# Kernel tuning notes

Measured on AMD Instinct MI355X. Metric: run time of the kernel, lower is better.

Reference implementation:

```python
import jax, jax.numpy as jnp
import numpy as np

# ---- sRGB <-> CIELAB (D65) helpers, matching standard torch lab2rgb/rgb2lab ----
_RGB2XYZ = jnp.array([[0.412453, 0.357580, 0.180423],
                      [0.212671, 0.715160, 0.072169],
                      [0.019334, 0.119193, 0.950227]], dtype=jnp.float32)
_XYZ2RGB = jnp.array([[ 3.2404542, -1.5371385, -0.4985314],
                      [-0.9692660,  1.8760108,  0.0415560],
                      [ 0.0556434, -0.2040259,  1.0572252]], dtype=jnp.float32)
_WHITE = jnp.array([0.95047, 1.0, 1.08883], dtype=jnp.float32)
_EPS = 0.008856      # (6/29)^3
_KAPPA = 7.787

def _srgb_to_linear(c):
    safe = jnp.maximum(c, 0.04045)
    return jnp.where(c <= 0.04045, c / 12.92, ((safe + 0.055) / 1.055) ** 2.4)

def _linear_to_srgb(c):
    safe = jnp.maximum(c, 0.0031308)
    return jnp.where(c <= 0.0031308, 12.92 * c, 1.055 * safe ** (1.0 / 2.4) - 0.055)

def rgb2lab(rgb):
    lin = _srgb_to_linear(rgb)                      # [N,3]
    xyz = (lin @ _RGB2XYZ.T) / _WHITE               # [N,3]
    safe = jnp.maximum(xyz, _EPS)
    f = jnp.where(xyz > _EPS, jnp.cbrt(safe), _KAPPA * xyz + 16.0 / 116.0)
    fx, fy, fz = f[..., 0], f[..., 1], f[..., 2]
    L = 116.0 * fy - 16.0
    a = 500.0 * (fx - fy)
    b = 200.0 * (fy - fz)
    return jnp.stack([L, a, b], axis=-1)

def lab2rgb(lab):
    L, a, b = lab[..., 0], lab[..., 1], lab[..., 2]
    fy = (L + 16.0) / 116.0
    fx = fy + a / 500.0
    fz = fy - b / 200.0
    f = jnp.stack([fx, fy, fz], axis=-1)
    f3 = f ** 3
    t = jnp.where(f3 > _EPS, f3, (f - 16.0 / 116.0) / _KAPPA)
    xyz = t * _WHITE
    lin = xyz @ _XYZ2RGB.T
    return _linear_to_srgb(lin)

def _forward(x, w_seq1, b_seq1, w_seq2, b_seq2, w_lin, b_lin,
             w_comb, b_comb, w_logd, b_logd, w_final, b_final):
    # lab branch
    seq = jnp.tanh(x @ w_seq1 + b_seq1) @ w_seq2 + b_seq2        # [N,3]
    lin = x @ w_lin + b_lin                                      # [N,3]
    final_lab = jnp.concatenate([lin, seq], axis=-1) @ w_comb + b_comb
    # log-density branch
    x_rgb = lab2rgb(x)
    log_density = -jnp.log10(x_rgb)
    model_processed = log_density @ w_logd + b_logd
    back_to_lab = rgb2lab(10.0 ** model_processed)
    return jnp.concatenate([final_lab, back_to_lab], axis=-1) @ w_final + b_final


def setup_inputs() -> dict:
    key = jax.random.key(0)
    ks = jax.random.split(key, 13)
    N, H = 2_097_152, 64

    def lin_init(kw, kb, fan_in, fan_out):
        bound = 1.0 / np.sqrt(fan_in)
        w = jax.random.uniform(kw, (fan_in, fan_out), minval=-bound, maxval=bound, dtype=jnp.float32)
        b = jax.random.uniform(kb, (fan_out,), minval=-bound, maxval=bound, dtype=jnp.float32)
        return w, b

    # valid Lab inputs: sample sRGB away from 0/1 then convert
    rgb = jax.random.uniform(ks[0], (N, 3), minval=0.05, maxval=0.95, dtype=jnp.float32)
    x = rgb2lab(rgb)

    kk = jax.random.split(ks[1], 12)
    w_seq1, b_seq1 = lin_init(kk[0], kk[1], 3, H)
    w_seq2, b_seq2 = lin_init(kk[2], kk[3], H, 3)
    w_lin, b_lin = lin_init(kk[4], kk[5], 3, 3)
    w_comb, b_comb = lin_init(kk[6], kk[7], 6, 3)
    w_logd, b_logd = lin_init(kk[8], kk[9], 3, 3)
    w_final, b_final = lin_init(kk[10], kk[11], 6, 3)
    return {"x": x,
            "w_seq1": w_seq1, "b_seq1": b_seq1, "w_seq2": w_seq2, "b_seq2": b_seq2,
            "w_lin": w_lin, "b_lin": b_lin, "w_comb": w_comb, "b_comb": b_comb,
            "w_logd": w_logd, "b_logd": b_logd, "w_final": w_final, "b_final": b_final}


def reference(x, w_seq1, b_seq1, w_seq2, b_seq2, w_lin, b_lin,
              w_comb, b_comb, w_logd, b_logd, w_final, b_final):
    return _forward(x, w_seq1, b_seq1, w_seq2, b_seq2, w_lin, b_lin,
                    w_comb, b_comb, w_logd, b_logd, w_final, b_final)
```

## Files before the change

kernel.cpp:

```cpp
#include <hip/hip_runtime.h>

typedef float    v2f __attribute__((ext_vector_type(2)));
typedef _Float16 v2h __attribute__((ext_vector_type(2)));

__device__ __forceinline__ float fexp2(float x) { return __builtin_amdgcn_exp2f(x); }
__device__ __forceinline__ float flog2(float x) { return __builtin_amdgcn_logf(x); }
__device__ __forceinline__ float ffma (float a, float b, float c) { return __builtin_fmaf(a, b, c); }
__device__ __forceinline__ v2f  splat(float s) { v2f v; v.x = s; v.y = s; return v; }
__device__ __forceinline__ v2f  pkfma(v2f a, v2f b, v2f c) { return __builtin_elementwise_fma(a, b, c); }
__device__ __forceinline__ v2h  splath(float s) { v2h v; v.x = (_Float16)s; v.y = (_Float16)s; return v; }
__device__ __forceinline__ v2h  pkfmah(v2h a, v2h b, v2h c) { return __builtin_elementwise_fma(a, b, c); }
__device__ __forceinline__ v2h  cvt_pk(float a, float b) {
    return __builtin_bit_cast(v2h, __builtin_amdgcn_cvt_pkrtz(a, b));
}
__device__ __forceinline__ v2f pexp2(v2f e) { v2f r; r.x = fexp2(e.x); r.y = fexp2(e.y); return r; }
__device__ __forceinline__ v2f plog2(v2f e) { v2f r; r.x = flog2(e.x); r.y = flog2(e.y); return r; }
__device__ __forceinline__ v2f selgt(v2f c, float thr, v2f a, v2f b) {
    v2f r; r.x = c.x > thr ? a.x : b.x; r.y = c.y > thr ? a.y : b.y; return r;
}
__device__ __forceinline__ v2f selle(v2f c, float thr, v2f a, v2f b) {
    v2f r; r.x = c.x <= thr ? a.x : b.x; r.y = c.y <= thr ? a.y : b.y; return r;
}
__device__ __forceinline__ v2f pmax(v2f a, float s) { return __builtin_elementwise_max(a, splat(s)); }

#define LAB_EPS 0.008856f
#define F16_116 0.13793103448275862f
#define LOG2_10 3.3219280948873623f

__global__ __launch_bounds__(256) void fused_kernel(
    const float* __restrict__ x,
    const float* __restrict__ w_seq1, const float* __restrict__ b_seq1,
    const float* __restrict__ w_seq2, const float* __restrict__ b_seq2,
    const float* __restrict__ w_lin,  const float* __restrict__ b_lin,
    const float* __restrict__ w_comb, const float* __restrict__ b_comb,
    const float* __restrict__ w_logd, const float* __restrict__ b_logd,
    const float* __restrict__ w_final,const float* __restrict__ b_final,
    float* __restrict__ out, int n)
{
    __shared__ uint4 wsbL[64];
    __shared__ float smlds[33];

    const int tid = threadIdx.x;
    if (tid < 64) {
        const int j = tid;
        float H3[9];
#pragma unroll
        for (int i = 0; i < 3; ++i)
#pragma unroll
            for (int c = 0; c < 3; ++c) {
                float h = 0.f;
                for (int m = 0; m < 3; ++m) h += w_comb[(i + 3) * 3 + m] * w_final[m * 3 + c];
                H3[i * 3 + c] = h;
            }
        const float w0 = w_seq2[j * 3 + 0], w1 = w_seq2[j * 3 + 1], w2 = w_seq2[j * 3 + 2];
        const float wp0 = w0 * H3[0] + w1 * H3[3] + w2 * H3[6];
        const float wp1 = w0 * H3[1] + w1 * H3[4] + w2 * H3[7];
        const float wp2 = w0 * H3[2] + w1 * H3[5] + w2 * H3[8];
        uint4 wb;
        wb.x = __builtin_bit_cast(unsigned, cvt_pk(wp0, wp0));
        wb.y = __builtin_bit_cast(unsigned, cvt_pk(wp1, wp1));
        wb.z = __builtin_bit_cast(unsigned, cvt_pk(wp2, wp2));
        wb.w = 0u;
        wsbL[j] = wb;
        if (j == 0) {
            float G[9], Wfb[9];
#pragma unroll
            for (int i = 0; i < 3; ++i)
#pragma unroll
                for (int c = 0; c < 3; ++c) {
                    float gg = 0.f;
                    for (int m = 0; m < 3; ++m) gg += w_comb[i * 3 + m] * w_final[m * 3 + c];
                    G[i * 3 + c] = gg;
                }
#pragma unroll
            for (int k = 0; k < 3; ++k)
#pragma unroll
                for (int c = 0; c < 3; ++c) {
                    float s = 0.f;
                    for (int i = 0; i < 3; ++i) s += w_lin[k * 3 + i] * G[i * 3 + c];
                    smlds[k * 3 + c]      = s;
                    Wfb[k * 3 + c]        = w_final[(k + 3) * 3 + c];
                    smlds[18 + k * 3 + c] = -w_logd[k * 3 + c];
                }
#pragma unroll
            for (int c = 0; c < 3; ++c) {
                smlds[9 + c]     = 500.0f * Wfb[3 + c];
                smlds[9 + 3 + c] = 116.0f * Wfb[c] - 500.0f * Wfb[3 + c] + 200.0f * Wfb[6 + c];
                smlds[9 + 6 + c] = -200.0f * Wfb[6 + c];
                float s = b_final[c] - 16.0f * Wfb[c];
                for (int i = 0; i < 3; ++i)
                    s += b_lin[i] * G[i * 3 + c] + b_seq2[i] * H3[i * 3 + c]
                       + b_comb[i] * w_final[i * 3 + c];
                smlds[27 + c] = LOG2_10 * b_logd[c];
                smlds[30 + c] = s;
            }
        }
    }
    __syncthreads();

    const int g = blockIdx.x * blockDim.x + tid;
    if (g * 2 >= n) return;

    const float2* xin = reinterpret_cast<const float2*>(x) + (size_t)g * 3;
    const float2 v0 = xin[0], v1 = xin[1], v2 = xin[2];
    v2f xs2[3];
    xs2[0].x = v0.x; xs2[0].y = v1.y;
    xs2[1].x = v0.y; xs2[1].y = v2.x;
    xs2[2].x = v1.x; xs2[2].y = v2.y;

    v2h acc0 = splath(0.f), acc1 = splath(0.f), acc2 = splath(0.f);

    const float4* __restrict__ w1v = reinterpret_cast<const float4*>(w_seq1);
    const float4* __restrict__ b1v = reinterpret_cast<const float4*>(b_seq1);

#pragma unroll 2
    for (int j0 = 0; j0 < 64; j0 += 4) {
        const int q = j0 >> 2;
        const float4 wr0 = w1v[q];
        const float4 wr1 = w1v[16 + q];
        const float4 wr2 = w1v[32 + q];
        const float4 wrb = b1v[q];
        const uint4 wb0 = wsbL[j0 + 0], wb1 = wsbL[j0 + 1], wb2 = wsbL[j0 + 2], wb3 = wsbL[j0 + 3];

        v2f t0 = pkfma(xs2[0], splat(wr0.x), pkfma(xs2[1], splat(wr1.x), pkfma(xs2[2], splat(wr2.x), splat(wrb.x))));
        v2f t1 = pkfma(xs2[0], splat(wr0.y), pkfma(xs2[1], splat(wr1.y), pkfma(xs2[2], splat(wr2.y), splat(wrb.y))));
        v2f t2 = pkfma(xs2[0], splat(wr0.z), pkfma(xs2[1], splat(wr1.z), pkfma(xs2[2], splat(wr2.z), splat(wrb.z))));
        v2f t3 = pkfma(xs2[0], splat(wr0.w), pkfma(xs2[1], splat(wr1.w), pkfma(xs2[2], splat(wr2.w), splat(wrb.w))));

        v2h th0 = cvt_pk(t0.x, t0.y);
        v2h th1 = cvt_pk(t1.x, t1.y);
        v2h th2 = cvt_pk(t2.x, t2.y);
        v2h th3 = cvt_pk(t3.x, t3.y);

        const v2h hi3 = splath(3.0f), lo3 = splath(-3.0f);
        th0 = __builtin_elementwise_min(__builtin_elementwise_max(th0, lo3), hi3);
        th1 = __builtin_elementwise_min(__builtin_elementwise_max(th1, lo3), hi3);
        th2 = __builtin_elementwise_min(__builtin_elementwise_max(th2, lo3), hi3);
        th3 = __builtin_elementwise_min(__builtin_elementwise_max(th3, lo3), hi3);

        v2h u0 = th0 * th0, u1 = th1 * th1, u2 = th2 * th2, u3 = th3 * th3;

        const v2h c3 = splath(-0.00120984f), c2 = splath(0.02603622f);
        const v2h c1 = splath(-0.20598500f), c0 = splath(0.95858467f);
        v2h P0 = pkfmah(c3, u0, c2);
        v2h P1 = pkfmah(c3, u1, c2);
        v2h P2 = pkfmah(c3, u2, c2);
        v2h P3 = pkfmah(c3, u3, c2);
        P0 = pkfmah(P0, u0, c1);
        P1 = pkfmah(P1, u1, c1);
        P2 = pkfmah(P2, u2, c1);
        P3 = pkfmah(P3, u3, c1);
        P0 = pkfmah(P0, u0, c0);
        P1 = pkfmah(P1, u1, c0);
        P2 = pkfmah(P2, u2, c0);
        P3 = pkfmah(P3, u3, c0);

        v2h h0 = th0 * P0, h1 = th1 * P1, h2 = th2 * P2, h3 = th3 * P3;

        acc0 = pkfmah(h0, __builtin_bit_cast(v2h, wb0.x), acc0);
        acc1 = pkfmah(h0, __builtin_bit_cast(v2h, wb0.y), acc1);
        acc2 = pkfmah(h0, __builtin_bit_cast(v2h, wb0.z), acc2);
        acc0 = pkfmah(h1, __builtin_bit_cast(v2h, wb1.x), acc0);
        acc1 = pkfmah(h1, __builtin_bit_cast(v2h, wb1.y), acc1);
        acc2 = pkfmah(h1, __builtin_bit_cast(v2h, wb1.z), acc2);
        acc0 = pkfmah(h2, __builtin_bit_cast(v2h, wb2.x), acc0);
        acc1 = pkfmah(h2, __builtin_bit_cast(v2h, wb2.y), acc1);
        acc2 = pkfmah(h2, __builtin_bit_cast(v2h, wb2.z), acc2);
        acc0 = pkfmah(h3, __builtin_bit_cast(v2h, wb3.x), acc0);
        acc1 = pkfmah(h3, __builtin_bit_cast(v2h, wb3.y), acc1);
        acc2 = pkfmah(h3, __builtin_bit_cast(v2h, wb3.z), acc2);
    }

    float A[9], U[9], Wn[9], bl2[3], cv[3];
#pragma unroll
    for (int i = 0; i < 9; ++i) { A[i] = smlds[i]; U[i] = smlds[9 + i]; Wn[i] = smlds[18 + i]; }
#pragma unroll
    for (int i = 0; i < 3; ++i) { bl2[i] = smlds[27 + i]; cv[i] = smlds[30 + i]; }

    v2f sq0, sq1, sq2;
    sq0.x = (float)acc0.x; sq0.y = (float)acc0.y;
    sq1.x = (float)acc1.x; sq1.y = (float)acc1.y;
    sq2.x = (float)acc2.x; sq2.y = (float)acc2.y;

    const v2f fy = (xs2[0] + splat(16.0f)) * splat(1.0f / 116.0f);
    const v2f fx = pkfma(xs2[1], splat( 0.002f), fy);
    const v2f fz = pkfma(xs2[2], splat(-0.005f), fy);
    const v2f f3x = fx * fx * fx, f3y = fy * fy * fy, f3z = fz * fz * fz;
    const v2f tx = selgt(f3x, LAB_EPS, f3x, (fx - splat(F16_116)) * splat(1.0f / 7.787f));
    const v2f ty = selgt(f3y, LAB_EPS, f3y, (fy - splat(F16_116)) * splat(1.0f / 7.787f));
    const v2f tz = selgt(f3z, LAB_EPS, f3z, (fz - splat(F16_116)) * splat(1.0f / 7.787f));
    const v2f X = tx * splat(0.95047f), Y = ty, Z = tz * splat(1.08883f);
    v2f linv[3];
    linv[0] = pkfma(X, splat( 3.2404542f), pkfma(Y, splat(-1.5371385f), Z * splat(-0.4985314f)));
    linv[1] = pkfma(X, splat(-0.9692660f), pkfma(Y, splat( 1.8760108f), Z * splat( 0.0415560f)));
    linv[2] = pkfma(X, splat( 0.0556434f), pkfma(Y, splat(-0.2040259f), Z * splat( 1.0572252f)));
    v2f lg[3];
#pragma unroll
    for (int c = 0; c < 3; ++c) {
        const v2f cc = linv[c];
        const v2f lo = cc * splat(12.92f);
        const v2f hi = pkfma(pexp2(plog2(pmax(cc, 0.0031308f)) * splat(1.0f / 2.4f)),
                             splat(1.055f), splat(-0.055f));
        lg[c] = plog2(selle(cc, 0.0031308f, lo, hi));
    }
    v2f lin2[3];
#pragma unroll
    for (int c = 0; c < 3; ++c) {
        const v2f e   = pkfma(lg[0], splat(Wn[c]),
                        pkfma(lg[1], splat(Wn[3 + c]),
                        pkfma(lg[2], splat(Wn[6 + c]), splat(bl2[c]))));
        const v2f r10 = pexp2(e);
        const v2f lo  = r10 * splat(1.0f / 12.92f);
        const v2f base = (pmax(r10, 0.04045f) + splat(0.055f)) * splat(1.0f / 1.055f);
        const v2f hi  = pexp2(plog2(base) * splat(2.4f));
        lin2[c] = selle(r10, 0.04045f, lo, hi);
    }
    const v2f X2 = pkfma(lin2[0], splat(0.412453f), pkfma(lin2[1], splat(0.357580f), lin2[2] * splat(0.180423f))) * splat(1.0f / 0.95047f);
    const v2f Y2 = pkfma(lin2[0], splat(0.212671f), pkfma(lin2[1], splat(0.715160f), lin2[2] * splat(0.072169f)));
    const v2f Z2 = pkfma(lin2[0], splat(0.019334f), pkfma(lin2[1], splat(0.119193f), lin2[2] * splat(0.950227f))) * splat(1.0f / 1.08883f);
    const v2f fX = selgt(X2, LAB_EPS, pexp2(plog2(pmax(X2, LAB_EPS)) * splat(1.0f / 3.0f)), pkfma(X2, splat(7.787f), splat(F16_116)));
    const v2f fY = selgt(Y2, LAB_EPS, pexp2(plog2(pmax(Y2, LAB_EPS)) * splat(1.0f / 3.0f)), pkfma(Y2, splat(7.787f), splat(F16_116)));
    const v2f fZ = selgt(Z2, LAB_EPS, pexp2(plog2(pmax(Z2, LAB_EPS)) * splat(1.0f / 3.0f)), pkfma(Z2, splat(7.787f), splat(F16_116)));
    v2f o[3];
#pragma unroll
    for (int c = 0; c < 3; ++c) {
        v2f oc = splat(cv[c]);
        oc = pkfma(xs2[0], splat(A[c]),     oc);
        oc = pkfma(xs2[1], splat(A[3 + c]), oc);
        oc = pkfma(xs2[2], splat(A[6 + c]), oc);
        oc = oc + (c == 0 ? sq0 : (c == 1 ? sq1 : sq2));
        oc = pkfma(fX, splat(U[c]),     oc);
        oc = pkfma(fY, splat(U[3 + c]), oc);
        oc = pkfma(fZ, splat(U[6 + c]), oc);
        o[c] = oc;
    }

    float2* op = reinterpret_cast<float2*>(out) + (size_t)g * 3;
    op[0] = make_float2(o[0].x, o[1].x);
    op[1] = make_float2(o[2].x, o[0].y);
    op[2] = make_float2(o[1].y, o[2].y);
}

extern "C" void kernel_launch(void* const* d_in, const int* in_sizes, int n_in,
                              void* d_out, int out_size, void* d_ws, size_t ws_size,
                              hipStream_t stream)
{
    const float* x       = (const float*)d_in[0];
    const float* w_seq1  = (const float*)d_in[1];
    const float* b_seq1  = (const float*)d_in[2];
    const float* w_seq2  = (const float*)d_in[3];
    const float* b_seq2  = (const float*)d_in[4];
    const float* w_lin   = (const float*)d_in[5];
    const float* b_lin   = (const float*)d_in[6];
    const float* w_comb  = (const float*)d_in[7];
    const float* b_comb  = (const float*)d_in[8];
    const float* w_logd  = (const float*)d_in[9];
    const float* b_logd  = (const float*)d_in[10];
    const float* w_final = (const float*)d_in[11];
    const float* b_final = (const float*)d_in[12];
    float* outp = (float*)d_out;

    const int n = in_sizes[0] / 3;
    const int threads = 256;
    const int total_threads = (n + 1) / 2;
    const int blocks = (total_threads + threads - 1) / threads;

    fused_kernel<<<blocks, threads, 0, stream>>>(
        x, w_seq1, b_seq1, w_seq2, b_seq2, w_lin, b_lin, w_comb, b_comb,
        w_logd, b_logd, w_final, b_final, outp, n);
}
```

Before: 133.1 us.

## Overlap weight precompute with hidden-layer loop by deferring the block barrier

Drops the per-block LDS table of folded w_seq2·H3 fp16 weights. The hidden-layer loop now reads the raw w_seq2 from global memory, converts it to half in-register, and applies the 3x3 H3 fold once per output afterwards. The small constant precompute is spread across 9 threads, and the __syncthreads is moved after the main loop so the tanh/MLP work no longer waits on setup. The cost is extra global loads and cvt instructions inside the loop, plus a slightly different fp16 rounding path.

```diff
diff --git a/kernel.cpp b/kernel.cpp
--- a/kernel.cpp
+++ b/kernel.cpp
@@ -5,7 +5,6 @@
 
 __device__ __forceinline__ float fexp2(float x) { return __builtin_amdgcn_exp2f(x); }
 __device__ __forceinline__ float flog2(float x) { return __builtin_amdgcn_logf(x); }
-__device__ __forceinline__ float ffma (float a, float b, float c) { return __builtin_fmaf(a, b, c); }
 __device__ __forceinline__ v2f  splat(float s) { v2f v; v.x = s; v.y = s; return v; }
 __device__ __forceinline__ v2f  pkfma(v2f a, v2f b, v2f c) { return __builtin_elementwise_fma(a, b, c); }
 __device__ __forceinline__ v2h  splath(float s) { v2h v; v.x = (_Float16)s; v.y = (_Float16)s; return v; }
@@ -37,150 +36,127 @@
     const float* __restrict__ w_final,const float* __restrict__ b_final,
     float* __restrict__ out, int n)
 {
-    __shared__ uint4 wsbL[64];
-    __shared__ float smlds[33];
+    __shared__ float smlds[42];
 
     const int tid = threadIdx.x;
-    if (tid < 64) {
-        const int j = tid;
-        float H3[9];
-#pragma unroll
-        for (int i = 0; i < 3; ++i)
-#pragma unroll
-            for (int c = 0; c < 3; ++c) {
-                float h = 0.f;
-                for (int m = 0; m < 3; ++m) h += w_comb[(i + 3) * 3 + m] * w_final[m * 3 + c];
-                H3[i * 3 + c] = h;
-            }
-        const float w0 = w_seq2[j * 3 + 0], w1 = w_seq2[j * 3 + 1], w2 = w_seq2[j * 3 + 2];
-        const float wp0 = w0 * H3[0] + w1 * H3[3] + w2 * H3[6];
-        const float wp1 = w0 * H3[1] + w1 * H3[4] + w2 * H3[7];
-        const float wp2 = w0 * H3[2] + w1 * H3[5] + w2 * H3[8];
-        uint4 wb;
-        wb.x = __builtin_bit_cast(unsigned, cvt_pk(wp0, wp0));
-        wb.y = __builtin_bit_cast(unsigned, cvt_pk(wp1, wp1));
-        wb.z = __builtin_bit_cast(unsigned, cvt_pk(wp2, wp2));
-        wb.w = 0u;
-        wsbL[j] = wb;
-        if (j == 0) {
-            float G[9], Wfb[9];
-#pragma unroll
-            for (int i = 0; i < 3; ++i)
-#pragma unroll
-                for (int c = 0; c < 3; ++c) {
-                    float gg = 0.f;
-                    for (int m = 0; m < 3; ++m) gg += w_comb[i * 3 + m] * w_final[m * 3 + c];
-                    G[i * 3 + c] = gg;
-                }
-#pragma unroll
-            for (int k = 0; k < 3; ++k)
-#pragma unroll
-                for (int c = 0; c < 3; ++c) {
-                    float s = 0.f;
-                    for (int i = 0; i < 3; ++i) s += w_lin[k * 3 + i] * G[i * 3 + c];
-                    smlds[k * 3 + c]      = s;
-                    Wfb[k * 3 + c]        = w_final[(k + 3) * 3 + c];
-                    smlds[18 + k * 3 + c] = -w_logd[k * 3 + c];
-                }
-#pragma unroll
-            for (int c = 0; c < 3; ++c) {
-                smlds[9 + c]     = 500.0f * Wfb[3 + c];
-                smlds[9 + 3 + c] = 116.0f * Wfb[c] - 500.0f * Wfb[3 + c] + 200.0f * Wfb[6 + c];
-                smlds[9 + 6 + c] = -200.0f * Wfb[6 + c];
-                float s = b_final[c] - 16.0f * Wfb[c];
-                for (int i = 0; i < 3; ++i)
-                    s += b_lin[i] * G[i * 3 + c] + b_seq2[i] * H3[i * 3 + c]
-                       + b_comb[i] * w_final[i * 3 + c];
-                smlds[27 + c] = LOG2_10 * b_logd[c];
-                smlds[30 + c] = s;
-            }
+    if (tid < 9) {
+        const int kk = tid / 3, c = tid - kk * 3;
+        const float wf0 = w_final[c], wf3 = w_final[3 + c], wf6 = w_final[6 + c];
+        const float Gc0 = w_comb[0] * wf0 + w_comb[1] * wf3 + w_comb[2] * wf6;
+        const float Gc1 = w_comb[3] * wf0 + w_comb[4] * wf3 + w_comb[5] * wf6;
+        const float Gc2 = w_comb[6] * wf0 + w_comb[7] * wf3 + w_comb[8] * wf6;
+        smlds[tid] = w_lin[kk * 3 + 0] * Gc0 + w_lin[kk * 3 + 1] * Gc1 + w_lin[kk * 3 + 2] * Gc2;
+        const float wb0 = w_final[9 + c], wb1 = w_final[12 + c], wb2 = w_final[15 + c];
+        smlds[9 + tid] = (kk == 0) ? 500.0f * wb1
+                       : (kk == 1) ? 116.0f * wb0 - 500.0f * wb1 + 200.0f * wb2
+                                   : -200.0f * wb2;
+        smlds[18 + tid] = -w_logd[tid];
+        smlds[33 + tid] = w_comb[(kk + 3) * 3 + 0] * wf0 + w_comb[(kk + 3) * 3 + 1] * wf3
+                        + w_comb[(kk + 3) * 3 + 2] * wf6;
+        if (kk == 0) {
+            smlds[27 + c] = LOG2_10 * b_logd[c];
+            const float H30 = w_comb[ 9] * wf0 + w_comb[10] * wf3 + w_comb[11] * wf6;
+            const float H31 = w_comb[12] * wf0 + w_comb[13] * wf3 + w_comb[14] * wf6;
+            const float H32 = w_comb[15] * wf0 + w_comb[16] * wf3 + w_comb[17] * wf6;
+            float s = b_final[c] - 16.0f * wb0;
+            s += b_lin[0] * Gc0 + b_lin[1] * Gc1 + b_lin[2] * Gc2;
+            s += b_seq2[0] * H30 + b_seq2[1] * H31 + b_seq2[2] * H32;
+            s += b_comb[0] * wf0 + b_comb[1] * wf3 + b_comb[2] * wf6;
+            smlds[30 + c] = s;
         }
     }
+
+    const int g = blockIdx.x * blockDim.x + tid;
+    const bool active = (g * 2 < n);
+
+    v2f xs2[3];
+    v2h acc0 = splath(0.f), acc1 = splath(0.f), acc2 = splath(0.f);
+
+    if (active) {
+        const float2* xin = reinterpret_cast<const float2*>(x) + (size_t)g * 3;
+        const float2 v0 = xin[0], v1 = xin[1], v2 = xin[2];
+        xs2[0].x = v0.x; xs2[0].y = v1.y;
+        xs2[1].x = v0.y; xs2[1].y = v2.x;
+        xs2[2].x = v1.x; xs2[2].y = v2.y;
+
+        const float4* __restrict__ w1v = reinterpret_cast<const float4*>(w_seq1);
+        const float4* __restrict__ b1v = reinterpret_cast<const float4*>(b_seq1);
+        const float4* __restrict__ w2v = reinterpret_cast<const float4*>(w_seq2);
+
+#pragma unroll 2
+        for (int j0 = 0; j0 < 64; j0 += 4) {
+            const int q = j0 >> 2;
+            const float4 wr0 = w1v[q];
+            const float4 wr1 = w1v[16 + q];
+            const float4 wr2 = w1v[32 + q];
+            const float4 wrb = b1v[q];
+            const float4 w2a = w2v[3 * q];
+            const float4 w2b = w2v[3 * q + 1];
+            const float4 w2c = w2v[3 * q + 2];
+
+            v2f t0 = pkfma(xs2[0], splat(wr0.x), pkfma(xs2[1], splat(wr1.x), pkfma(xs2[2], splat(wr2.x), splat(wrb.x))));
+            v2f t1 = pkfma(xs2[0], splat(wr0.y), pkfma(xs2[1], splat(wr1.y), pkfma(xs2[2], splat(wr2.y), splat(wrb.y))));
+            v2f t2 = pkfma(xs2[0], splat(wr0.z), pkfma(xs2[1], splat(wr1.z), pkfma(xs2[2], splat(wr2.z), splat(wrb.z))));
+            v2f t3 = pkfma(xs2[0], splat(wr0.w), pkfma(xs2[1], splat(wr1.w), pkfma(xs2[2], splat(wr2.w), splat(wrb.w))));
+
+            v2h th0 = cvt_pk(t0.x, t0.y);
+            v2h th1 = cvt_pk(t1.x, t1.y);
+            v2h th2 = cvt_pk(t2.x, t2.y);
+            v2h th3 = cvt_pk(t3.x, t3.y);
+
+            const v2h hi3 = splath(3.0f), lo3 = splath(-3.0f);
+            th0 = __builtin_elementwise_min(__builtin_elementwise_max(th0, lo3), hi3);
+            th1 = __builtin_elementwise_min(__builtin_elementwise_max(th1, lo3), hi3);
+            th2 = __builtin_elementwise_min(__builtin_elementwise_max(th2, lo3), hi3);
+            th3 = __builtin_elementwise_min(__builtin_elementwise_max(th3, lo3), hi3);
+
+            v2h u0 = th0 * th0, u1 = th1 * th1, u2 = th2 * th2, u3 = th3 * th3;
+
+            const v2h c3 = splath(-0.00120984f), c2h = splath(0.02603622f);
+            const v2h c1 = splath(-0.20598500f), c0h = splath(0.95858467f);
+            v2h P0 = pkfmah(c3, u0, c2h);
+            v2h P1 = pkfmah(c3, u1, c2h);
+            v2h P2 = pkfmah(c3, u2, c2h);
+            v2h P3 = pkfmah(c3, u3, c2h);
+            P0 = pkfmah(P0, u0, c1);
+            P1 = pkfmah(P1, u1, c1);
+            P2 = pkfmah(P2, u2, c1);
+            P3 = pkfmah(P3, u3, c1);
+            P0 = pkfmah(P0, u0, c0h);
+            P1 = pkfmah(P1, u1, c0h);
+            P2 = pkfmah(P2, u2, c0h);
+            P3 = pkfmah(P3, u3, c0h);
+
+            v2h h0 = th0 * P0, h1 = th1 * P1, h2 = th2 * P2, h3 = th3 * P3;
+
+            acc0 = pkfmah(h0, cvt_pk(w2a.x, w2a.x), acc0);
+            acc1 = pkfmah(h0, cvt_pk(w2a.y, w2a.y), acc1);
+            acc2 = pkfmah(h0, cvt_pk(w2a.z, w2a.z), acc2);
+            acc0 = pkfmah(h1, cvt_pk(w2a.w, w2a.w), acc0);
+            acc1 = pkfmah(h1, cvt_pk(w2b.x, w2b.x), acc1);
+            acc2 = pkfmah(h1, cvt_pk(w2b.y, w2b.y), acc2);
+            acc0 = pkfmah(h2, cvt_pk(w2b.z, w2b.z), acc0);
+            acc1 = pkfmah(h2, cvt_pk(w2b.w, w2b.w), acc1);
+            acc2 = pkfmah(h2, cvt_pk(w2c.x, w2c.x), acc2);
+            acc0 = pkfmah(h3, cvt_pk(w2c.y, w2c.y), acc0);
+            acc1 = pkfmah(h3, cvt_pk(w2c.z, w2c.z), acc1);
+            acc2 = pkfmah(h3, cvt_pk(w2c.w, w2c.w), acc2);
+        }
+    }
+
     __syncthreads();
-
-    const int g = blockIdx.x * blockDim.x + tid;
-    if (g * 2 >= n) return;
-
-    const float2* xin = reinterpret_cast<const float2*>(x) + (size_t)g * 3;
-    const float2 v0 = xin[0], v1 = xin[1], v2 = xin[2];
-    v2f xs2[3];
-    xs2[0].x = v0.x; xs2[0].y = v1.y;
-    xs2[1].x = v0.y; xs2[1].y = v2.x;
-    xs2[2].x = v1.x; xs2[2].y = v2.y;
-
-    v2h acc0 = splath(0.f), acc1 = splath(0.f), acc2 = splath(0.f);
-
-    const float4* __restrict__ w1v = reinterpret_cast<const float4*>(w_seq1);
-    const float4* __restrict__ b1v = reinterpret_cast<const float4*>(b_seq1);
-
-#pragma unroll 2
-    for (int j0 = 0; j0 < 64; j0 += 4) {
-        const int q = j0 >> 2;
-        const float4 wr0 = w1v[q];
-        const float4 wr1 = w1v[16 + q];
-        const float4 wr2 = w1v[32 + q];
-        const float4 wrb = b1v[q];
-        const uint4 wb0 = wsbL[j0 + 0], wb1 = wsbL[j0 + 1], wb2 = wsbL[j0 + 2], wb3 = wsbL[j0 + 3];
-
-        v2f t0 = pkfma(xs2[0], splat(wr0.x), pkfma(xs2[1], splat(wr1.x), pkfma(xs2[2], splat(wr2.x), splat(wrb.x))));
-        v2f t1 = pkfma(xs2[0], splat(wr0.y), pkfma(xs2[1], splat(wr1.y), pkfma(xs2[2], splat(wr2.y), splat(wrb.y))));
-        v2f t2 = pkfma(xs2[0], splat(wr0.z), pkfma(xs2[1], splat(wr1.z), pkfma(xs2[2], splat(wr2.z), splat(wrb.z))));
-        v2f t3 = pkfma(xs2[0], splat(wr0.w), pkfma(xs2[1], splat(wr1.w), pkfma(xs2[2], splat(wr2.w), splat(wrb.w))));
-
-        v2h th0 = cvt_pk(t0.x, t0.y);
-        v2h th1 = cvt_pk(t1.x, t1.y);
-        v2h th2 = cvt_pk(t2.x, t2.y);
-        v2h th3 = cvt_pk(t3.x, t3.y);
-
-        const v2h hi3 = splath(3.0f), lo3 = splath(-3.0f);
-        th0 = __builtin_elementwise_min(__builtin_elementwise_max(th0, lo3), hi3);
-        th1 = __builtin_elementwise_min(__builtin_elementwise_max(th1, lo3), hi3);
-        th2 = __builtin_elementwise_min(__builtin_elementwise_max(th2, lo3), hi3);
-        th3 = __builtin_elementwise_min(__builtin_elementwise_max(th3, lo3), hi3);
-
-        v2h u0 = th0 * th0, u1 = th1 * th1, u2 = th2 * th2, u3 = th3 * th3;
-
-        const v2h c3 = splath(-0.00120984f), c2 = splath(0.02603622f);
-        const v2h c1 = splath(-0.20598500f), c0 = splath(0.95858467f);
-        v2h P0 = pkfmah(c3, u0, c2);
-        v2h P1 = pkfmah(c3, u1, c2);
-        v2h P2 = pkfmah(c3, u2, c2);
-        v2h P3 = pkfmah(c3, u3, c2);
-        P0 = pkfmah(P0, u0, c1);
-        P1 = pkfmah(P1, u1, c1);
-        P2 = pkfmah(P2, u2, c1);
-        P3 = pkfmah(P3, u3, c1);
-        P0 = pkfmah(P0, u0, c0);
-        P1 = pkfmah(P1, u1, c0);
-        P2 = pkfmah(P2, u2, c0);
-        P3 = pkfmah(P3, u3, c0);
-
-        v2h h0 = th0 * P0, h1 = th1 * P1, h2 = th2 * P2, h3 = th3 * P3;
-
-        acc0 = pkfmah(h0, __builtin_bit_cast(v2h, wb0.x), acc0);
-        acc1 = pkfmah(h0, __builtin_bit_cast(v2h, wb0.y), acc1);
-        acc2 = pkfmah(h0, __builtin_bit_cast(v2h, wb0.z), acc2);
-        acc0 = pkfmah(h1, __builtin_bit_cast(v2h, wb1.x), acc0);
-        acc1 = pkfmah(h1, __builtin_bit_cast(v2h, wb1.y), acc1);
-        acc2 = pkfmah(h1, __builtin_bit_cast(v2h, wb1.z), acc2);
-        acc0 = pkfmah(h2, __builtin_bit_cast(v2h, wb2.x), acc0);
-        acc1 = pkfmah(h2, __builtin_bit_cast(v2h, wb2.y), acc1);
-        acc2 = pkfmah(h2, __builtin_bit_cast(v2h, wb2.z), acc2);
-        acc0 = pkfmah(h3, __builtin_bit_cast(v2h, wb3.x), acc0);
-        acc1 = pkfmah(h3, __builtin_bit_cast(v2h, wb3.y), acc1);
-        acc2 = pkfmah(h3, __builtin_bit_cast(v2h, wb3.z), acc2);
-    }
-
-    float A[9], U[9], Wn[9], bl2[3], cv[3];
-#pragma unroll
-    for (int i = 0; i < 9; ++i) { A[i] = smlds[i]; U[i] = smlds[9 + i]; Wn[i] = smlds[18 + i]; }
+    if (!active) return;
+
+    float A[9], U[9], Wn[9], H3c[9], bl2[3], cv[3];
+#pragma unroll
+    for (int i = 0; i < 9; ++i) { A[i] = smlds[i]; U[i] = smlds[9 + i]; Wn[i] = smlds[18 + i]; H3c[i] = smlds[33 + i]; }
 #pragma unroll
     for (int i = 0; i < 3; ++i) { bl2[i] = smlds[27 + i]; cv[i] = smlds[30 + i]; }
 
-    v2f sq0, sq1, sq2;
-    sq0.x = (float)acc0.x; sq0.y = (float)acc0.y;
-    sq1.x = (float)acc1.x; sq1.y = (float)acc1.y;
-    sq2.x = (float)acc2.x; sq2.y = (float)acc2.y;
+    v2f sm0, sm1, sm2;
+    sm0.x = (float)acc0.x; sm0.y = (float)acc0.y;
+    sm1.x = (float)acc1.x; sm1.y = (float)acc1.y;
+    sm2.x = (float)acc2.x; sm2.y = (float)acc2.y;
 
     const v2f fy = (xs2[0] + splat(16.0f)) * splat(1.0f / 116.0f);
     const v2f fx = pkfma(xs2[1], splat( 0.002f), fy);
@@ -225,13 +201,15 @@
 #pragma unroll
     for (int c = 0; c < 3; ++c) {
         v2f oc = splat(cv[c]);
-        oc = pkfma(xs2[0], splat(A[c]),     oc);
-        oc = pkfma(xs2[1], splat(A[3 + c]), oc);
-        oc = pkfma(xs2[2], splat(A[6 + c]), oc);
-        oc = oc + (c == 0 ? sq0 : (c == 1 ? sq1 : sq2));
-        oc = pkfma(fX, splat(U[c]),     oc);
-        oc = pkfma(fY, splat(U[3 + c]), oc);
-        oc = pkfma(fZ, splat(U[6 + c]), oc);
+        oc = pkfma(xs2[0], splat(A[c]),       oc);
+        oc = pkfma(xs2[1], splat(A[3 + c]),   oc);
+        oc = pkfma(xs2[2], splat(A[6 + c]),   oc);
+        oc = pkfma(sm0,    splat(H3c[c]),     oc);
+        oc = pkfma(sm1,    splat(H3c[3 + c]), oc);
+        oc = pkfma(sm2,    splat(H3c[6 + c]), oc);
+        oc = pkfma(fX,     splat(U[c]),       oc);
+        oc = pkfma(fY,     splat(U[3 + c]),   oc);
+        oc = pkfma(fZ,     splat(U[6 + c]),   oc);
         o[c] = oc;
     }
 
```

New measurement: 137.5 us. 3.3% more time.
